# Kernel tuning notes

Measured on AMD Instinct MI355X. Metric: run time of the kernel, lower is better.

Reference implementation:

```python
import jax, jax.numpy as jnp
import numpy as np

N = 1_000_000
VOCAB = 50_000
EMBED_DIM = 128
ENCODE_DIM = 128


def _random_preorder_tree(n, seed=0):
    """Generate a random tree whose nodes are numbered in pre-order DFS.
    Returns subtree_end[i] = index of the last node in node i's subtree (inclusive)."""
    rng = np.random.default_rng(seed)
    parent = np.empty(n, dtype=np.int64)
    parent[0] = -1
    stack = [0]
    pops = rng.geometric(0.5, size=n) - 1  # how far up to climb before attaching
    for i in range(1, n):
        npop = min(int(pops[i]), len(stack) - 1)
        for _ in range(npop):
            stack.pop()
        parent[i] = stack[-1]
        stack.append(i)
    end = np.arange(n, dtype=np.int64)
    for i in range(n - 1, 0, -1):
        p = parent[i]
        if end[p] < end[i]:
            end[p] = end[i]
    return end


def setup_inputs() -> dict:
    key = jax.random.key(0)
    k1, k2, k3, k4 = jax.random.split(key, 4)
    tokens = jax.random.randint(k1, (N,), 0, VOCAB, dtype=jnp.int64).astype(jnp.int32)
    subtree_end = jnp.asarray(_random_preorder_tree(N), dtype=jnp.int32)
    embedding_weight = jax.random.normal(k2, (VOCAB, EMBED_DIM), dtype=jnp.float32)
    W = jax.random.normal(k3, (ENCODE_DIM, EMBED_DIM), dtype=jnp.float32) * (1.0 / np.sqrt(EMBED_DIM))
    b = jax.random.normal(k4, (ENCODE_DIM,), dtype=jnp.float32) * 0.01
    return {"tokens": tokens, "subtree_end": subtree_end,
            "embedding_weight": embedding_weight, "W": W, "b": b}


def reference(tokens, subtree_end, embedding_weight, W, b):
    # Per-node contribution: x_i = Linear(Embed(token_i))          [N, encode_dim]
    x = embedding_weight[tokens] @ W.T + b
    # h_i = sum of x over subtree(i). With pre-order DFS numbering, the subtree
    # of i is the contiguous range [i, subtree_end[i]], so use an inclusive
    # prefix sum: h_i = S[end_i] - S[i] + x_i.
    S = jnp.cumsum(x, axis=0)                                      # [N, encode_dim]
    h = S[subtree_end] - S + x                                     # [N, encode_dim]
    # pool = max over all node hidden states (order-independent)
    return jnp.max(h, axis=0)                                      # [encode_dim]
```

## Files before the change

### kernel.cpp

```cpp
#include <hip/hip_runtime.h>
#include <hip/hip_bf16.h>

#define D      128
#define LG     9
#define CHUNK  512

typedef __attribute__((ext_vector_type(8))) short          short8;
typedef __attribute__((ext_vector_type(8))) unsigned short ushort8;
typedef __attribute__((ext_vector_type(4))) float          floatx4;
typedef __attribute__((ext_vector_type(2))) float          floatx2;

__device__ inline float b2f(unsigned short u) {
    return __uint_as_float(((unsigned)u) << 16);
}
__device__ inline unsigned short f2bf(float f) {
    __hip_bfloat16 h = __float2bfloat16(f);
    unsigned short u;
    __builtin_memcpy(&u, &h, 2);
    return u;
}
__device__ inline short8 u2s(ushort8 u) {
    short8 s; __builtin_memcpy(&s, &u, 16); return s;
}
__device__ inline void atomicMaxF(float* addr, float v) {
    if (v >= 0.f) atomicMax((int*)addr, __float_as_int(v));
    else          atomicMin((unsigned int*)addr, __float_as_uint(v));
}

__global__ void init_out_kernel(float* out, int out_size) {
    int t = threadIdx.x;
    if (t < out_size) out[t] = -INFINITY;
}

__global__ __launch_bounds__(128) void local_scan_kernel(
        const int* __restrict__ tokens, const float* __restrict__ emb,
        unsigned* __restrict__ T32, float* __restrict__ sumE, int n, int C) {
    __shared__ int toks[2][CHUNK];
    int tid = threadIdx.x, w = tid >> 6, lane = tid & 63;
    int cb = min(blockIdx.x * 2 + w, C - 1);
    int i0 = cb << LG, cnt = min(CHUNK, n - i0);
    for (int t = lane; t < cnt; t += 64) toks[w][t] = tokens[i0 + t];
    __syncthreads();
    const floatx2* eb = (const floatx2*)emb;
    float rx = 0.f, ry = 0.f;
    unsigned* To = T32 + (size_t)i0 * 64 + lane;
    #pragma unroll 4
    for (int j = 0; j < cnt; ++j) {
        floatx2 v = eb[(size_t)toks[w][j] * 64 + lane];
        rx += v[0]; ry += v[1];
        unsigned pk = ((unsigned)f2bf(rx)) | (((unsigned)f2bf(ry)) << 16);
        __builtin_nontemporal_store(pk, To + (size_t)j * 64);
    }
    floatx2 rr = {rx, ry};
    *(floatx2*)(sumE + (size_t)cb * D + lane * 2) = rr;
}

__global__ void scan_kernel(float* sumE, unsigned short* prefB, int C) {
    int d    = blockIdx.x;
    int lane = threadIdx.x;
    float carry = 0.f;
    for (int c0 = 0; c0 < C; c0 += 64) {
        int c = c0 + lane;
        float v = (c < C) ? sumE[(size_t)c * D + d] : 0.f;
        float incl = v;
        #pragma unroll
        for (int off = 1; off < 64; off <<= 1) {
            float t = __shfl_up(incl, off);
            if (lane >= off) incl += t;
        }
        if (c < C) {
            float exc = carry + incl - v;
            sumE[(size_t)c * D + d] = exc;
            prefB[(size_t)c * D + d] = f2bf(exc);
        }
        carry += __shfl(incl, 63);
    }
}

__global__ __launch_bounds__(256, 2) void max_pass_kernel(
        const int* __restrict__ ends, const unsigned short* __restrict__ S,
        const unsigned short* __restrict__ prefB, const float* __restrict__ W,
        const float* __restrict__ bvec, float* __restrict__ out,
        int n, int tpw) {
    __shared__ float red[4][4][16];
    int tid = threadIdx.x, lane = tid & 63, wid = tid >> 6;
    int c  = lane & 15;
    int kg = lane >> 4;
    int tw = wid & 1;
    int pr = wid >> 1;

    short8 Wf[4][4];
    float  bc[4];
    #pragma unroll
    for (int tl = 0; tl < 4; ++tl) {
        const float* wr = W + (size_t)((tw * 4 + tl) * 16 + c) * D + kg * 8;
        bc[tl] = bvec[(tw * 4 + tl) * 16 + c];
        #pragma unroll
        for (int kk = 0; kk < 4; ++kk) {
            floatx4 f0 = *(const floatx4*)(wr + kk * 32);
            floatx4 f1 = *(const floatx4*)(wr + kk * 32 + 4);
            short8 w;
            #pragma unroll
            for (int j = 0; j < 4; ++j) { w[j] = (short)f2bf(f0[j]); w[j + 4] = (short)f2bf(f1[j]); }
            Wf[tl][kk] = w;
        }
    }
    float mx[4];
    #pragma unroll
    for (int tl = 0; tl < 4; ++tl) mx[tl] = -INFINITY;

    const ushort8* Sv = (const ushort8*)S;
    const ushort8* PB = (const ushort8*)prefB;
    int gp = blockIdx.x * 2 + pr;
    int STRIDE = gridDim.x * 2;
    ushort8 zero8 = {0, 0, 0, 0, 0, 0, 0, 0};

#define TIDX(k)  (gp + (k) * STRIDE)
#define LD_E(k)  ends[min(TIDX(k) * 16 + c, n - 1)]
#define LOAD_EROWS(k, e, QE, SE) do {                                    \
        int ce_ = (e) >> LG;                                             \
        const ushort8* se_ = Sv + (size_t)(e) * 16 + kg;                 \
        const ushort8* qe_ = PB + (size_t)ce_ * 16 + kg;                 \
        SE[0] = se_[0]; SE[1] = se_[4]; SE[2] = se_[8]; SE[3] = se_[12]; \
        QE[0] = qe_[0]; QE[1] = qe_[4]; QE[2] = qe_[8]; QE[3] = qe_[12]; \
    } while (0)

#define PROCESS(k, e, QE, SE) do {                                       \
        int base_ = TIDX(k) * 16;                                        \
        int node_ = base_ + c;                                           \
        int pc_ = max(min(node_, n) - 1, 0);                             \
        int cp_ = pc_ >> LG;                                             \
        const ushort8* sp_ = Sv + (size_t)pc_ * 16 + kg;                 \
        const ushort8* qp_ = PB + (size_t)cp_ * 16 + kg;                 \
        ushort8 SP[4], QP[4];                                            \
        SP[0] = sp_[0]; SP[1] = sp_[4]; SP[2] = sp_[8]; SP[3] = sp_[12]; \
        QP[0] = qp_[0]; QP[1] = qp_[4]; QP[2] = qp_[8]; QP[3] = qp_[12]; \
        if (node_ == 0) { SP[0] = zero8; SP[1] = zero8; SP[2] = zero8; SP[3] = zero8; } \
        floatx4 cnt4_;                                                   \
        _Pragma("unroll")                                                \
        for (int i = 0; i < 4; ++i)                                      \
            cnt4_[i] = (float)(__shfl((e), kg * 4 + i) - (base_ + kg * 4 + i) + 1); \
        _Pragma("unroll")                                                \
        for (int tl = 0; tl < 4; ++tl) {                                 \
            floatx4 ae_ = {0.f, 0.f, 0.f, 0.f};                          \
            floatx4 ap_ = {0.f, 0.f, 0.f, 0.f};                          \
            _Pragma("unroll")                                            \
            for (int kk = 0; kk < 4; ++kk) {                             \
                ae_ = __builtin_amdgcn_mfma_f32_16x16x32_bf16(u2s(QE[kk]), Wf[tl][kk], ae_, 0, 0, 0); \
                ap_ = __builtin_amdgcn_mfma_f32_16x16x32_bf16(u2s(QP[kk]), Wf[tl][kk], ap_, 0, 0, 0); \
            }                                                            \
            _Pragma("unroll")                                            \
            for (int kk = 0; kk < 4; ++kk) {                             \
                ae_ = __builtin_amdgcn_mfma_f32_16x16x32_bf16(u2s(SE[kk]), Wf[tl][kk], ae_, 0, 0, 0); \
                ap_ = __builtin_amdgcn_mfma_f32_16x16x32_bf16(u2s(SP[kk]), Wf[tl][kk], ap_, 0, 0, 0); \
            }                                                            \
            _Pragma("unroll")                                            \
            for (int i = 0; i < 4; ++i) {                                \
                float h_ = (ae_[i] - ap_[i]) + cnt4_[i] * bc[tl];        \
                if (base_ + kg * 4 + i < n) mx[tl] = fmaxf(mx[tl], h_);  \
            }                                                            \
        }                                                                \
    } while (0)

    ushort8 QEa[4], SEa[4], QEb[4], SEb[4];
    int e0 = LD_E(0);
    LOAD_EROWS(0, e0, QEa, SEa);
    int e1 = LD_E(1);
    for (int k = 0; k < tpw; k += 2) {
        LOAD_EROWS(k + 1, e1, QEb, SEb);
        int e2 = LD_E(k + 2);
        PROCESS(k, e0, QEa, SEa);
        LOAD_EROWS(k + 2, e2, QEa, SEa);
        int e3 = LD_E(k + 3);
        PROCESS(k + 1, e1, QEb, SEb);
        e0 = e2; e1 = e3;
    }

    #pragma unroll
    for (int tl = 0; tl < 4; ++tl) {
        float v = mx[tl];
        v = fmaxf(v, __shfl_xor(v, 16));
        v = fmaxf(v, __shfl_xor(v, 32));
        mx[tl] = v;
    }
    if (kg == 0) {
        #pragma unroll
        for (int tl = 0; tl < 4; ++tl) red[wid][tl][c] = mx[tl];
    }
    __syncthreads();
    if (tid < 128) {
        int twf = tid >> 6;
        int tl  = (tid >> 4) & 3;
        int cc  = tid & 15;
        float v = fmaxf(red[twf][tl][cc], red[twf + 2][tl][cc]);
        atomicMaxF(&out[(twf * 4 + tl) * 16 + cc], v);
    }
}

extern "C" void kernel_launch(void* const* d_in, const int* in_sizes, int n_in,
                              void* d_out, int out_size, void* d_ws, size_t ws_size,
                              hipStream_t stream) {
    const int*   tokens = (const int*)d_in[0];
    const int*   ends   = (const int*)d_in[1];
    const float* emb    = (const float*)d_in[2];
    const float* W      = (const float*)d_in[3];
    const float* bvec   = (const float*)d_in[4];
    float* out = (float*)d_out;
    int n = in_sizes[0];
    int C = (n + CHUNK - 1) >> LG;

    unsigned short* S     = (unsigned short*)d_ws;
    float*          sumE  = (float*)(S + (size_t)n * D);
    unsigned short* prefB = (unsigned short*)(sumE + (size_t)C * D);

    init_out_kernel<<<1, 128, 0, stream>>>(out, out_size);
    local_scan_kernel<<<(C + 1) / 2, 128, 0, stream>>>(tokens, emb,
                                                       (unsigned*)S, sumE, n, C);
    scan_kernel<<<128, 64, 0, stream>>>(sumE, prefB, C);

    int n_tiles = (n + 15) / 16;
    int nblocks = 512;
    int pairs   = nblocks * 2;
    int tpw = ((n_tiles + pairs - 1) / pairs + 1) & ~1;
    max_pass_kernel<<<nblocks, 256, 0, stream>>>(ends, S, prefB, W, bvec, out,
                                                 n, tpw);
}
```

Baseline: 273.0 us.

## Precompute W-projected chunk prefixes to skip predecessor-prefix MFMAs in interior tiles

Adds a small kernel that multiplies the fp32 chunk exclusive prefix sums by W, giving per-chunk projected offsets. In the max pass, tiles that sit inside a chunk and away from the array end subtract this precomputed fp32 value instead of loading the bf16 predecessor prefix row and running four extra MFMAs per output tile. Boundary tiles keep the old path. The intent is to cut loads and matrix work in the hot loop. The cost is an extra kernel launch and a divergent branch, and the fp32 offset rounds differently from the bf16 one.

```diff
diff --git a/kernel.cpp b/kernel.cpp
--- a/kernel.cpp
+++ b/kernel.cpp
@@ -77,11 +77,32 @@
     }
 }
 
+__global__ __launch_bounds__(128) void wp_kernel(
+        const float* __restrict__ W, float* __restrict__ P, int C) {
+    __shared__ float pl[16][D];
+    int d = threadIdx.x;
+    int c0 = blockIdx.x * 16;
+    int nr = min(16, C - c0);
+    for (int r = 0; r < nr; ++r) pl[r][d] = P[(size_t)(c0 + r) * D + d];
+    __syncthreads();
+    float acc[16];
+    #pragma unroll
+    for (int r = 0; r < 16; ++r) acc[r] = 0.f;
+    const float* wr = W + (size_t)d * D;
+    for (int k = 0; k < D; ++k) {
+        float wk = wr[k];
+        #pragma unroll
+        for (int r = 0; r < 16; ++r) acc[r] += wk * pl[r][k];
+    }
+    __syncthreads();
+    for (int r = 0; r < nr; ++r) P[(size_t)(c0 + r) * D + d] = acc[r];
+}
+
 __global__ __launch_bounds__(256, 2) void max_pass_kernel(
         const int* __restrict__ ends, const unsigned short* __restrict__ S,
-        const unsigned short* __restrict__ prefB, const float* __restrict__ W,
-        const float* __restrict__ bvec, float* __restrict__ out,
-        int n, int tpw) {
+        const unsigned short* __restrict__ prefB, const float* __restrict__ WP,
+        const float* __restrict__ W, const float* __restrict__ bvec,
+        float* __restrict__ out, int n, int tpw) {
     __shared__ float red[4][4][16];
     int tid = threadIdx.x, lane = tid & 63, wid = tid >> 6;
     int c  = lane & 15;
@@ -129,35 +150,61 @@
         int base_ = TIDX(k) * 16;                                        \
         int node_ = base_ + c;                                           \
         int pc_ = max(min(node_, n) - 1, 0);                             \
-        int cp_ = pc_ >> LG;                                             \
         const ushort8* sp_ = Sv + (size_t)pc_ * 16 + kg;                 \
-        const ushort8* qp_ = PB + (size_t)cp_ * 16 + kg;                 \
-        ushort8 SP[4], QP[4];                                            \
+        ushort8 SP[4];                                                   \
         SP[0] = sp_[0]; SP[1] = sp_[4]; SP[2] = sp_[8]; SP[3] = sp_[12]; \
-        QP[0] = qp_[0]; QP[1] = qp_[4]; QP[2] = qp_[8]; QP[3] = qp_[12]; \
-        if (node_ == 0) { SP[0] = zero8; SP[1] = zero8; SP[2] = zero8; SP[3] = zero8; } \
         floatx4 cnt4_;                                                   \
         _Pragma("unroll")                                                \
         for (int i = 0; i < 4; ++i)                                      \
             cnt4_[i] = (float)(__shfl((e), kg * 4 + i) - (base_ + kg * 4 + i) + 1); \
-        _Pragma("unroll")                                                \
-        for (int tl = 0; tl < 4; ++tl) {                                 \
-            floatx4 ae_ = {0.f, 0.f, 0.f, 0.f};                          \
-            floatx4 ap_ = {0.f, 0.f, 0.f, 0.f};                          \
+        if ((base_ & (CHUNK - 1)) != 0 && base_ + 15 < n) {              \
+             \
+            const float* wpr_ = WP + (size_t)(base_ >> LG) * D + c;      \
             _Pragma("unroll")                                            \
-            for (int kk = 0; kk < 4; ++kk) {                             \
-                ae_ = __builtin_amdgcn_mfma_f32_16x16x32_bf16(u2s(QE[kk]), Wf[tl][kk], ae_, 0, 0, 0); \
-                ap_ = __builtin_amdgcn_mfma_f32_16x16x32_bf16(u2s(QP[kk]), Wf[tl][kk], ap_, 0, 0, 0); \
+            for (int tl = 0; tl < 4; ++tl) {                             \
+                float wps_ = wpr_[(tw * 4 + tl) * 16];                   \
+                floatx4 ae_ = {0.f, 0.f, 0.f, 0.f};                      \
+                floatx4 ap_ = {0.f, 0.f, 0.f, 0.f};                      \
+                _Pragma("unroll")                                        \
+                for (int kk = 0; kk < 4; ++kk) {                         \
+                    ae_ = __builtin_amdgcn_mfma_f32_16x16x32_bf16(u2s(QE[kk]), Wf[tl][kk], ae_, 0, 0, 0); \
+                    ap_ = __builtin_amdgcn_mfma_f32_16x16x32_bf16(u2s(SP[kk]), Wf[tl][kk], ap_, 0, 0, 0); \
+                }                                                        \
+                _Pragma("unroll")                                        \
+                for (int kk = 0; kk < 4; ++kk)                           \
+                    ae_ = __builtin_amdgcn_mfma_f32_16x16x32_bf16(u2s(SE[kk]), Wf[tl][kk], ae_, 0, 0, 0); \
+                _Pragma("unroll")                                        \
+                for (int i = 0; i < 4; ++i) {                            \
+                    float h_ = (ae_[i] - ap_[i]) - wps_ + cnt4_[i] * bc[tl]; \
+                    mx[tl] = fmaxf(mx[tl], h_);                          \
+                }                                                        \
             }                                                            \
+        } else {                                                         \
+                            \
+            int cp_ = pc_ >> LG;                                         \
+            const ushort8* qp_ = PB + (size_t)cp_ * 16 + kg;             \
+            ushort8 QP[4];                                               \
+            QP[0] = qp_[0]; QP[1] = qp_[4]; QP[2] = qp_[8]; QP[3] = qp_[12]; \
+            if (node_ == 0) { SP[0] = zero8; SP[1] = zero8; SP[2] = zero8; SP[3] = zero8; } \
             _Pragma("unroll")                                            \
-            for (int kk = 0; kk < 4; ++kk) {                             \
-                ae_ = __builtin_amdgcn_mfma_f32_16x16x32_bf16(u2s(SE[kk]), Wf[tl][kk], ae_, 0, 0, 0); \
-                ap_ = __builtin_amdgcn_mfma_f32_16x16x32_bf16(u2s(SP[kk]), Wf[tl][kk], ap_, 0, 0, 0); \
-            }                                                            \
-            _Pragma("unroll")                                            \
-            for (int i = 0; i < 4; ++i) {                                \
-                float h_ = (ae_[i] - ap_[i]) + cnt4_[i] * bc[tl];        \
-                if (base_ + kg * 4 + i < n) mx[tl] = fmaxf(mx[tl], h_);  \
+            for (int tl = 0; tl < 4; ++tl) {                             \
+                floatx4 ae_ = {0.f, 0.f, 0.f, 0.f};                      \
+                floatx4 ap_ = {0.f, 0.f, 0.f, 0.f};                      \
+                _Pragma("unroll")                                        \
+                for (int kk = 0; kk < 4; ++kk) {                         \
+                    ae_ = __builtin_amdgcn_mfma_f32_16x16x32_bf16(u2s(QE[kk]), Wf[tl][kk], ae_, 0, 0, 0); \
+                    ap_ = __builtin_amdgcn_mfma_f32_16x16x32_bf16(u2s(QP[kk]), Wf[tl][kk], ap_, 0, 0, 0); \
+                }                                                        \
+                _Pragma("unroll")                                        \
+                for (int kk = 0; kk < 4; ++kk) {                         \
+                    ae_ = __builtin_amdgcn_mfma_f32_16x16x32_bf16(u2s(SE[kk]), Wf[tl][kk], ae_, 0, 0, 0); \
+                    ap_ = __builtin_amdgcn_mfma_f32_16x16x32_bf16(u2s(SP[kk]), Wf[tl][kk], ap_, 0, 0, 0); \
+                }                                                        \
+                _Pragma("unroll")                                        \
+                for (int i = 0; i < 4; ++i) {                            \
+                    float h_ = (ae_[i] - ap_[i]) + cnt4_[i] * bc[tl];    \
+                    if (base_ + kg * 4 + i < n) mx[tl] = fmaxf(mx[tl], h_); \
+                }                                                        \
             }                                                            \
         }                                                                \
     } while (0)
@@ -217,11 +264,12 @@
     local_scan_kernel<<<(C + 1) / 2, 128, 0, stream>>>(tokens, emb,
                                                        (unsigned*)S, sumE, n, C);
     scan_kernel<<<128, 64, 0, stream>>>(sumE, prefB, C);
+    wp_kernel<<<(C + 15) / 16, 128, 0, stream>>>(W, sumE, C);
 
     int n_tiles = (n + 15) / 16;
     int nblocks = 512;
     int pairs   = nblocks * 2;
     int tpw = ((n_tiles + pairs - 1) / pairs + 1) & ~1;
-    max_pass_kernel<<<nblocks, 256, 0, stream>>>(ends, S, prefB, W, bvec, out,
-                                                 n, tpw);
-}
+    max_pass_kernel<<<nblocks, 256, 0, stream>>>(ends, S, prefB, sumE, W, bvec,
+                                                 out, n, tpw);
+}
```

Measured after the change: 278.6 us. +2.1%, slower.
